# Performance work log

Hardware: AMD Instinct MI355X
Metric: run time of the kernel (lower is better)

## Reference

```python
import jax, jax.numpy as jnp
import numpy as np

N_NODES = 100000
N_EDGES = 600000
VOCAB = 5000
NUM_GRAPHS = 2000
NUM_CLASSES = 10


def setup_inputs() -> dict:
    key = jax.random.key(0)
    ks = jax.random.split(key, 12)
    x = jax.random.randint(ks[0], (N_NODES,), 0, VOCAB, dtype=jnp.int32)
    edge_index = jax.random.randint(ks[1], (2, N_EDGES), 0, N_NODES, dtype=jnp.int32)
    batch = jnp.sort(jax.random.randint(ks[2], (N_NODES,), 0, NUM_GRAPHS, dtype=jnp.int32))
    emb = jax.random.normal(ks[3], (VOCAB, 64), dtype=jnp.float32) * 0.1
    W1 = jax.random.normal(ks[4], (64, 128), dtype=jnp.float32) * (1.0 / np.sqrt(64))
    b1 = jnp.zeros((128,), dtype=jnp.float32)
    W2 = jax.random.normal(ks[5], (128, 128), dtype=jnp.float32) * (1.0 / np.sqrt(128))
    b2 = jnp.zeros((128,), dtype=jnp.float32)
    Wlin = jax.random.normal(ks[6], (128, NUM_CLASSES), dtype=jnp.float32) * (1.0 / np.sqrt(128))
    blin = jnp.zeros((NUM_CLASSES,), dtype=jnp.float32)
    return {"x": x, "edge_index": edge_index, "batch": batch, "num_graphs": NUM_GRAPHS,
            "emb": emb, "W1": W1, "b1": b1, "W2": W2, "b2": b2, "Wlin": Wlin, "blin": blin}


def reference(x, edge_index, batch, num_graphs, emb, W1, b1, W2, b2, Wlin, blin):
    N = x.shape[0]
    loops = jnp.arange(N, dtype=edge_index.dtype)
    src = jnp.concatenate([edge_index[0], loops])  # message sources (j)
    dst = jnp.concatenate([edge_index[1], loops])  # aggregation targets (i)
    # GCN symmetric normalization with self-loops (PyG gcn_norm, source_to_target)
    deg = jax.ops.segment_sum(jnp.ones_like(dst, dtype=jnp.float32), dst, num_segments=N)
    dinv = jnp.where(deg > 0, jax.lax.rsqrt(deg), 0.0)
    norm = dinv[src] * dinv[dst]  # [E+N]

    def gcn(h, W, b):
        h = h @ W  # linear transform first (GCNConv order)
        msg = h[src] * norm[:, None]  # gather + scale, [E+N, F]
        return jax.ops.segment_sum(msg, dst, num_segments=N) + b

    h = emb[x]  # [N, 64]
    h = jax.nn.relu(gcn(h, W1, b1))
    h = jax.nn.relu(gcn(h, W2, b2))
    g = jax.ops.segment_max(h, batch, num_segments=num_graphs)  # global_max_pool
    return g @ Wlin + blin
```

## Files before the change

### kernel.cpp

```cpp
#include <hip/hip_runtime.h>
#include <hip/hip_bf16.h>
#include <hip/hip_fp16.h>


typedef _Float16 h8 __attribute__((ext_vector_type(8)));
typedef _Float16 h4v __attribute__((ext_vector_type(4)));
typedef float f32x4 __attribute__((ext_vector_type(4)));

__global__ __launch_bounds__(256) void k_zero(int4* __restrict__ deg4, int n4i,
                                              int4* __restrict__ pool4, int p4i,
                                              int4* __restrict__ xpad, int x4i) {
    int t = blockIdx.x * 256 + threadIdx.x;
    int4 z = make_int4(0, 0, 0, 0);
    if (t < n4i) deg4[t] = z;
    if (t < p4i) pool4[t] = z;
    if (t < x4i) xpad[t] = z;
}

__global__ __launch_bounds__(256) void k_degprep(const int* __restrict__ dst, int* __restrict__ deg, int E,
                                                 const float* __restrict__ emb, __half2* __restrict__ e16,
                                                 const float* __restrict__ W1, _Float16* __restrict__ W1T,
                                                 const float* __restrict__ W2, _Float16* __restrict__ W2T,
                                                 int nEmbF, int gE, int nCast) {
    int bid = blockIdx.x;
    if (bid < gE) {
        int e = bid * 256 + threadIdx.x;
        if (e < E) atomicAdd(&deg[dst[e]], 1);
    } else if (bid < gE + nCast) {
        int t = (bid - gE) * 256 + threadIdx.x;
        if (t * 4 < nEmbF) {
            float4 v = *(const float4*)&emb[t * 4];
            e16[t * 2] = __floats2half2_rn(v.x, v.y);
            e16[t * 2 + 1] = __floats2half2_rn(v.z, v.w);
        }
    } else if (bid < gE + nCast + 32) {
        int t = (bid - gE - nCast) * 256 + threadIdx.x;
        int c = t >> 6, k = t & 63;
        W1T[c * 64 + k] = (_Float16)W1[k * 128 + c];
    } else {
        int t = (bid - gE - nCast - 32) * 256 + threadIdx.x;
        if (t < 128 * 128) {
            int c = t >> 7, k = t & 127;
            W2T[c * 128 + k] = (_Float16)W2[k * 128 + c];
        }
    }
}

__global__ __launch_bounds__(256) void k_scan1(const int* __restrict__ deg, int* __restrict__ exc,
                                               int* __restrict__ bsums, float* __restrict__ dinv, int N) {
    __shared__ int s[256];
    int i = blockIdx.x * 256 + threadIdx.x;
    int v = (i < N) ? deg[i] : 0;
    if (i < N) dinv[i] = rsqrtf((float)(v + 1));
    s[threadIdx.x] = v;
    __syncthreads();
    for (int off = 1; off < 256; off <<= 1) {
        int t = (threadIdx.x >= (unsigned)off) ? s[threadIdx.x - off] : 0;
        __syncthreads();
        s[threadIdx.x] += t;
        __syncthreads();
    }
    if (i < N) exc[i] = s[threadIdx.x] - v;
    if (threadIdx.x == 255) bsums[blockIdx.x] = s[255];
}

__global__ __launch_bounds__(512) void k_scan2(int* __restrict__ bsums, int nb) {
    __shared__ int s[512];
    int i = threadIdx.x;
    int v = (i < nb) ? bsums[i] : 0;
    s[i] = v;
    __syncthreads();
    for (int off = 1; off < 512; off <<= 1) {
        int t = (i >= off) ? s[i - off] : 0;
        __syncthreads();
        s[i] += t;
        __syncthreads();
    }
    if (i < nb) bsums[i] = s[i] - v;
}

__global__ __launch_bounds__(256) void k_scan3(int* __restrict__ rowstart, int* __restrict__ cursor,
                                               const int* __restrict__ bsums, int N, int E) {
    int i = blockIdx.x * 256 + threadIdx.x;
    if (i < N) {
        int r = rowstart[i] + bsums[blockIdx.x];
        rowstart[i] = r;
        cursor[i] = r;
    }
    if (i == 0 && blockIdx.x == 0) rowstart[N] = E;
}

__global__ __launch_bounds__(256) void k_fill(const int* __restrict__ src, const int* __restrict__ dst,
                                              const int* __restrict__ x, const float* __restrict__ dinv,
                                              int* __restrict__ cursor, int4* __restrict__ rec, int E) {
    int e = blockIdx.x * 256 + threadIdx.x;
    if (e < E) {
        int d = dst[e];
        int s = src[e];
        int pos = atomicAdd(&cursor[d], 1);
        rec[pos] = make_int4(x[s], __float_as_int(dinv[s]), s, 0);
    }
}

__global__ __launch_bounds__(256) void k_agge(const __half2* __restrict__ e16, const int* __restrict__ x,
                                              const float* __restrict__ dinv, const int* __restrict__ rs,
                                              const int4* __restrict__ rec, __half2* __restrict__ Xagg, int N) {
    int lane = threadIdx.x & 31;
    int n0 = (blockIdx.x * 8 + (threadIdx.x >> 5)) * 2;
    if (n0 >= N) return;
    int nB = (n0 + 1 < N) ? n0 + 1 : n0;
    int cA0 = rs[n0], cA1 = rs[n0 + 1];
    int cB0 = rs[nB], cB1 = rs[nB + 1];
    bool hasA = cA0 < cA1, hasB = cB0 < cB1;
    __half2 tA[8], tB[8];
    float wA[8], wB[8];
#pragma unroll
    for (int i = 0; i < 8; ++i) {
        int ei = cA0 + i;
        int ec = (ei < cA1) ? ei : (hasA ? cA1 - 1 : 0);
        int4 r2 = rec[ec];
        tA[i] = e16[(size_t)r2.x * 32 + lane];
        wA[i] = (ei < cA1) ? __int_as_float(r2.y) : 0.f;
    }
#pragma unroll
    for (int i = 0; i < 8; ++i) {
        int ei = cB0 + i;
        int ec = (ei < cB1) ? ei : (hasB ? cB1 - 1 : 0);
        int4 r2 = rec[ec];
        tB[i] = e16[(size_t)r2.x * 32 + lane];
        wB[i] = (ei < cB1) ? __int_as_float(r2.y) : 0.f;
    }
    float dA = dinv[n0], dB = dinv[nB];
    float2 sA = __half22float2(e16[(size_t)x[n0] * 32 + lane]);
    float2 sB = __half22float2(e16[(size_t)x[nB] * 32 + lane]);
    float aA0 = dA * sA.x, aA1 = dA * sA.y;
    float aB0 = dB * sB.x, aB1 = dB * sB.y;
#pragma unroll
    for (int i = 0; i < 8; ++i) {
        float2 tf = __half22float2(tA[i]);
        aA0 = fmaf(wA[i], tf.x, aA0);
        aA1 = fmaf(wA[i], tf.y, aA1);
    }
#pragma unroll
    for (int i = 0; i < 8; ++i) {
        float2 tf = __half22float2(tB[i]);
        aB0 = fmaf(wB[i], tf.x, aB0);
        aB1 = fmaf(wB[i], tf.y, aB1);
    }
    for (int e = cA0 + 8; e < cA1; e += 8) {
#pragma unroll
        for (int i = 0; i < 8; ++i) {
            int ei = e + i;
            int ec = (ei < cA1) ? ei : cA1 - 1;
            int4 r2 = rec[ec];
            tA[i] = e16[(size_t)r2.x * 32 + lane];
            wA[i] = (ei < cA1) ? __int_as_float(r2.y) : 0.f;
        }
#pragma unroll
        for (int i = 0; i < 8; ++i) {
            float2 tf = __half22float2(tA[i]);
            aA0 = fmaf(wA[i], tf.x, aA0);
            aA1 = fmaf(wA[i], tf.y, aA1);
        }
    }
    for (int e = cB0 + 8; e < cB1; e += 8) {
#pragma unroll
        for (int i = 0; i < 8; ++i) {
            int ei = e + i;
            int ec = (ei < cB1) ? ei : cB1 - 1;
            int4 r2 = rec[ec];
            tB[i] = e16[(size_t)r2.x * 32 + lane];
            wB[i] = (ei < cB1) ? __int_as_float(r2.y) : 0.f;
        }
#pragma unroll
        for (int i = 0; i < 8; ++i) {
            float2 tf = __half22float2(tB[i]);
            aB0 = fmaf(wB[i], tf.x, aB0);
            aB1 = fmaf(wB[i], tf.y, aB1);
        }
    }
    Xagg[(size_t)n0 * 32 + lane] = __floats2half2_rn(dA * aA0, dA * aA1);
    Xagg[(size_t)nB * 32 + lane] = __floats2half2_rn(dB * aB0, dB * aB1);
}

__global__ __launch_bounds__(256) void k_gemm12(const _Float16* __restrict__ Xagg,
                                                const _Float16* __restrict__ W1T, const float* __restrict__ b1,
                                                const _Float16* __restrict__ W2T, const float* __restrict__ dinv,
                                                _Float16* __restrict__ P, int N) {
    __shared__ _Float16 Hs[64][136];
    int tid = threadIdx.x;
    int l = tid & 63, wid = tid >> 6;
    int r = l & 15, kg = l >> 4;
    int blk0 = blockIdx.x * 64;
    {
        f32x4 acc[8];
#pragma unroll
        for (int ct = 0; ct < 8; ++ct) acc[ct] = (f32x4){0.f, 0.f, 0.f, 0.f};
        const _Float16* ab = Xagg + (size_t)(blk0 + wid * 16 + r) * 64 + kg * 8;
#pragma unroll
        for (int kc = 0; kc < 2; ++kc) {
            h8 a = *(const h8*)(ab + kc * 32);
#pragma unroll
            for (int ct = 0; ct < 8; ++ct) {
                h8 b = *(const h8*)(W1T + (size_t)(ct * 16 + r) * 64 + kc * 32 + kg * 8);
                acc[ct] = __builtin_amdgcn_mfma_f32_16x16x32_f16(a, b, acc[ct], 0, 0, 0);
            }
        }
#pragma unroll
        for (int ct = 0; ct < 8; ++ct) {
            float bias = b1[ct * 16 + r];
#pragma unroll
            for (int i = 0; i < 4; ++i)
                Hs[wid * 16 + 4 * kg + i][ct * 16 + r] = (_Float16)fmaxf(acc[ct][i] + bias, 0.f);
        }
    }
    __syncthreads();
    {
        f32x4 acc[8];
#pragma unroll
        for (int ct = 0; ct < 8; ++ct) acc[ct] = (f32x4){0.f, 0.f, 0.f, 0.f};
#pragma unroll
        for (int kc = 0; kc < 4; ++kc) {
            h8 a = *(const h8*)&Hs[wid * 16 + r][kc * 32 + kg * 8];
#pragma unroll
            for (int ct = 0; ct < 8; ++ct) {
                h8 b = *(const h8*)(W2T + (size_t)(ct * 16 + r) * 128 + kc * 32 + kg * 8);
                acc[ct] = __builtin_amdgcn_mfma_f32_16x16x32_f16(a, b, acc[ct], 0, 0, 0);
            }
        }
        float dv[4];
#pragma unroll
        for (int i = 0; i < 4; ++i) {
            int gr = blk0 + wid * 16 + 4 * kg + i;
            dv[i] = (gr < N) ? dinv[gr] : 0.f;
        }
#pragma unroll
        for (int ct = 0; ct < 8; ++ct) {
#pragma unroll
            for (int i = 0; i < 4; ++i) {
                int gr = blk0 + wid * 16 + 4 * kg + i;
                if (gr < N) P[(size_t)gr * 128 + ct * 16 + r] = (_Float16)(acc[ct][i] * dv[i]);
            }
        }
    }
}

__global__ __launch_bounds__(256) void k_agg2pool(const h4v* __restrict__ P4, const int* __restrict__ batch,
                                                  const float* __restrict__ dinv, const int* __restrict__ rs,
                                                  const int4* __restrict__ rec, const float4* __restrict__ bias4,
                                                  float* __restrict__ pool, int N, int G) {
    __shared__ int lpool[4][128];
    int tid = threadIdx.x;
    lpool[tid >> 7][tid & 127] = 0;
    lpool[(tid >> 7) + 2][tid & 127] = 0;
    __syncthreads();
    int lane = tid & 31;
    int blk_n0 = blockIdx.x * 16;
    int gfirst = batch[(blk_n0 < N) ? blk_n0 : (N - 1)];
    int n0 = blk_n0 + (tid >> 5) * 2;
    if (n0 < N) {
        int nA = n0;
        int nB = (n0 + 1 < N) ? n0 + 1 : n0;
        int cA0 = rs[nA], cA1 = rs[nA + 1];
        int cB0 = rs[nB], cB1 = rs[nB + 1];
        bool hasA = cA0 < cA1, hasB = cB0 < cB1;
        h4v sA = P4[(size_t)nA * 32 + lane];
        h4v sB = P4[(size_t)nB * 32 + lane];
        float aA[4], aB[4];
#pragma unroll
        for (int f = 0; f < 4; ++f) {
            aA[f] = (float)sA[f];
            aB[f] = (float)sB[f];
        }
        {
            h4v tA[16], tB[16];
#pragma unroll
            for (int i = 0; i < 16; ++i) {
                int ei = cA0 + i;
                int ec = (ei < cA1) ? ei : (hasA ? cA1 - 1 : 0);
                tA[i] = P4[(size_t)rec[ec].z * 32 + lane];
            }
#pragma unroll
            for (int i = 0; i < 16; ++i) {
                int ei = cB0 + i;
                int ec = (ei < cB1) ? ei : (hasB ? cB1 - 1 : 0);
                tB[i] = P4[(size_t)rec[ec].z * 32 + lane];
            }
#pragma unroll
            for (int i = 0; i < 16; ++i) {
                float w = (cA0 + i < cA1) ? 1.f : 0.f;
#pragma unroll
                for (int f = 0; f < 4; ++f) aA[f] = fmaf(w, (float)tA[i][f], aA[f]);
            }
#pragma unroll
            for (int i = 0; i < 16; ++i) {
                float w = (cB0 + i < cB1) ? 1.f : 0.f;
#pragma unroll
                for (int f = 0; f < 4; ++f) aB[f] = fmaf(w, (float)tB[i][f], aB[f]);
            }
        }
        for (int e = cA0 + 16; e < cA1; e += 16) {
            h4v t[16];
#pragma unroll
            for (int i = 0; i < 16; ++i) {
                int ei = e + i;
                int ec = (ei < cA1) ? ei : cA1 - 1;
                t[i] = P4[(size_t)rec[ec].z * 32 + lane];
            }
#pragma unroll
            for (int i = 0; i < 16; ++i) {
                float w = (e + i < cA1) ? 1.f : 0.f;
#pragma unroll
                for (int f = 0; f < 4; ++f) aA[f] = fmaf(w, (float)t[i][f], aA[f]);
            }
        }
        for (int e = cB0 + 16; e < cB1; e += 16) {
            h4v t[16];
#pragma unroll
            for (int i = 0; i < 16; ++i) {
                int ei = e + i;
                int ec = (ei < cB1) ? ei : cB1 - 1;
                t[i] = P4[(size_t)rec[ec].z * 32 + lane];
            }
#pragma unroll
            for (int i = 0; i < 16; ++i) {
                float w = (e + i < cB1) ? 1.f : 0.f;
#pragma unroll
                for (int f = 0; f < 4; ++f) aB[f] = fmaf(w, (float)t[i][f], aB[f]);
            }
        }
        float dA = dinv[nA], dB = dinv[nB];
        int gA = batch[nA], gB = batch[nB];
        float4 b = bias4[lane];
        float bv[4] = {b.x, b.y, b.z, b.w};
        float zA[4], zB[4];
#pragma unroll
        for (int f = 0; f < 4; ++f) {
            zA[f] = fmaxf(fmaf(dA, aA[f], bv[f]), 0.f);
            zB[f] = fmaxf(fmaf(dB, aB[f], bv[f]), 0.f);
        }
        int rot = (lane >> 3) & 3;
        auto emit = [&](int g, const float* m) {
            int slot = g - gfirst;
            if (slot < 4) {
#pragma unroll
                for (int f = 0; f < 4; ++f) {
                    int ff = (f + rot) & 3;
                    if (m[ff] > 0.f) atomicMax(&lpool[slot][lane * 4 + ff], __float_as_int(m[ff]));
                }
            } else {
                float* pg = pool + (size_t)g * 128 + lane * 4;
#pragma unroll
                for (int f = 0; f < 4; ++f)
                    if (m[f] > 0.f) atomicMax((int*)(pg + f), __float_as_int(m[f]));
            }
        };
        if (gA == gB) {
            float m[4];
#pragma unroll
            for (int f = 0; f < 4; ++f) m[f] = fmaxf(zA[f], zB[f]);
            emit(gA, m);
        } else {
            emit(gA, zA);
            emit(gB, zB);
        }
    }
    __syncthreads();
    {
        int f = tid & 127;
        for (int s = tid >> 7; s < 4; s += 2) {
            int v = lpool[s][f];
            if (v > 0) atomicMax((int*)&pool[(size_t)(gfirst + s) * 128 + f], v);
        }
    }
}

__global__ __launch_bounds__(256) void k_final(const float* __restrict__ pool, const float* __restrict__ Wlin,
                                               const float* __restrict__ blin, float* __restrict__ out, int G) {
    int t = blockIdx.x * 256 + threadIdx.x;
    if (t >= G * 10) return;
    int g = t / 10, c = t % 10;
    float acc = blin[c];
    const float* pr = pool + (size_t)g * 128;
#pragma unroll 8
    for (int f = 0; f < 128; ++f) acc = fmaf(pr[f], Wlin[f * 10 + c], acc);
    out[t] = acc;
}

extern "C" void kernel_launch(void* const* d_in, const int* in_sizes, int n_in,
                              void* d_out, int out_size, void* d_ws, size_t ws_size,
                              hipStream_t stream) {
    const int* x = (const int*)d_in[0];
    const int* ei = (const int*)d_in[1];
    const int* batch = (const int*)d_in[2];
    const float* emb = (const float*)d_in[4];
    const float* W1 = (const float*)d_in[5];
    const float* b1 = (const float*)d_in[6];
    const float* W2 = (const float*)d_in[7];
    const float* b2 = (const float*)d_in[8];
    const float* Wlin = (const float*)d_in[9];
    const float* blin = (const float*)d_in[10];
    float* out = (float*)d_out;

    int N = in_sizes[0];
    int E = in_sizes[1] / 2;
    int VOCAB = in_sizes[4] / 64;
    int G = out_size / 10;
    const int* srcp = ei;
    const int* dstp = ei + E;

    char* p = (char*)d_ws;
    auto alloc = [&](size_t bytes) -> char* {
        char* r = p;
        p += (bytes + 255) & ~(size_t)255;
        return r;
    };
    int Npad = (N + 63) & ~63;
    int* deg = (int*)alloc((size_t)N * 4);
    int* cursor = (int*)alloc((size_t)N * 4);
    int* rowstart = (int*)alloc((size_t)(N + 1) * 4);
    int* bsums = (int*)alloc(512 * 4);
    float* dinv = (float*)alloc((size_t)N * 4);
    int4* rec = (int4*)alloc((size_t)E * 16);
    _Float16* e16 = (_Float16*)alloc((size_t)VOCAB * 64 * 2);
    _Float16* W1T = (_Float16*)alloc(128 * 64 * 2);
    _Float16* W2T = (_Float16*)alloc(128 * 128 * 2);
    _Float16* Xagg = (_Float16*)alloc((size_t)Npad * 64 * 2);
    _Float16* P = (_Float16*)alloc((size_t)N * 128 * 2);
    float* pool = (float*)alloc((size_t)G * 128 * 4);

    int gE = (E + 255) / 256;
    int gN = (N + 255) / 256;
    int nEmbF = VOCAB * 64;
    int nCast = (nEmbF / 4 + 255) / 256;

    int n4i = N / 4, p4i = G * 128 / 4;
    int x4i = (Npad - N) * 64 * 2 / 16;
    int zmax = n4i > p4i ? n4i : p4i;
    k_zero<<<(zmax + 255) / 256, 256, 0, stream>>>((int4*)deg, n4i, (int4*)pool, p4i,
                                                   (int4*)(Xagg + (size_t)N * 64), x4i);
    k_degprep<<<gE + nCast + 32 + 64, 256, 0, stream>>>(dstp, deg, E, emb, (__half2*)e16, W1, W1T,
                                                        W2, W2T, nEmbF, gE, nCast);
    k_scan1<<<gN, 256, 0, stream>>>(deg, rowstart, bsums, dinv, N);
    k_scan2<<<1, 512, 0, stream>>>(bsums, gN);
    k_scan3<<<gN, 256, 0, stream>>>(rowstart, cursor, bsums, N, E);
    k_fill<<<gE, 256, 0, stream>>>(srcp, dstp, x, dinv, cursor, rec, E);
    k_agge<<<(N + 15) / 16, 256, 0, stream>>>((const __half2*)e16, x, dinv, rowstart, rec,
                                              (__half2*)Xagg, N);
    k_gemm12<<<(N + 63) / 64, 256, 0, stream>>>(Xagg, W1T, b1, W2T, dinv, P, N);
    k_agg2pool<<<(N + 15) / 16, 256, 0, stream>>>((const h4v*)P, batch, dinv, rowstart, rec,
                                                  (const float4*)b2, pool, N, G);
    k_final<<<(G * 10 + 255) / 256, 256, 0, stream>>>(pool, Wlin, blin, out, G);
}
```

Before: 197.6 us.

## Reorder layer-2 as aggregate-then-transform and fuse W2 GEMM into pooling kernel

Layer 2 now aggregates the relu'd layer-1 activations h1 over neighbours first and applies the W2 MFMA GEMM afterwards, inside the same kernel that does bias, relu and global max pooling. k_gemm1 now only computes layer 1 and writes h1 through shared memory with coalesced stores. Previously W2 was applied per node before aggregation, producing an intermediate P. The fused kernel uses per-row gathers across lanes in MFMA layout with a __any-driven edge loop, two edges per step, and uses 8 shared pooling slots instead of 4. The gather is now unbalanced across rows within a wavefront, and its access pattern is less coalesced than the old lane-per-feature gather.

```diff
diff --git a/kernel.cpp b/kernel.cpp
--- a/kernel.cpp
+++ b/kernel.cpp
@@ -4,7 +4,6 @@
 
 
 typedef _Float16 h8 __attribute__((ext_vector_type(8)));
-typedef _Float16 h4v __attribute__((ext_vector_type(4)));
 typedef float f32x4 __attribute__((ext_vector_type(4)));
 
 __global__ __launch_bounds__(256) void k_zero(int4* __restrict__ deg4, int n4i,
@@ -183,195 +182,138 @@
     Xagg[(size_t)nB * 32 + lane] = __floats2half2_rn(dB * aB0, dB * aB1);
 }
 
-__global__ __launch_bounds__(256) void k_gemm12(const _Float16* __restrict__ Xagg,
-                                                const _Float16* __restrict__ W1T, const float* __restrict__ b1,
-                                                const _Float16* __restrict__ W2T, const float* __restrict__ dinv,
-                                                _Float16* __restrict__ P, int N) {
+__global__ __launch_bounds__(256) void k_gemm1(const _Float16* __restrict__ Xagg,
+                                               const _Float16* __restrict__ W1T,
+                                               const float* __restrict__ b1,
+                                               _Float16* __restrict__ h1, int Npad) {
     __shared__ _Float16 Hs[64][136];
     int tid = threadIdx.x;
     int l = tid & 63, wid = tid >> 6;
     int r = l & 15, kg = l >> 4;
     int blk0 = blockIdx.x * 64;
+    f32x4 acc[8];
+#pragma unroll
+    for (int ct = 0; ct < 8; ++ct) acc[ct] = (f32x4){0.f, 0.f, 0.f, 0.f};
+    const _Float16* ab = Xagg + (size_t)(blk0 + wid * 16 + r) * 64 + kg * 8;
+#pragma unroll
+    for (int kc = 0; kc < 2; ++kc) {
+        h8 a = *(const h8*)(ab + kc * 32);
+#pragma unroll
+        for (int ct = 0; ct < 8; ++ct) {
+            h8 b = *(const h8*)(W1T + (size_t)(ct * 16 + r) * 64 + kc * 32 + kg * 8);
+            acc[ct] = __builtin_amdgcn_mfma_f32_16x16x32_f16(a, b, acc[ct], 0, 0, 0);
+        }
+    }
+#pragma unroll
+    for (int ct = 0; ct < 8; ++ct) {
+        float bias = b1[ct * 16 + r];
+#pragma unroll
+        for (int i = 0; i < 4; ++i)
+            Hs[wid * 16 + 4 * kg + i][ct * 16 + r] = (_Float16)fmaxf(acc[ct][i] + bias, 0.f);
+    }
+    __syncthreads();
+    int row = tid >> 2, q = tid & 3;
+    const int4* srcp = (const int4*)&Hs[row][q * 32];
+    int4 v0 = srcp[0], v1 = srcp[1], v2 = srcp[2], v3 = srcp[3];
+    int4* dst = (int4*)(h1 + (size_t)(blk0 + row) * 128 + q * 32);
+    dst[0] = v0; dst[1] = v1; dst[2] = v2; dst[3] = v3;
+}
+
+#define SLOTS 8
+__global__ __launch_bounds__(256) void k_aggpool(const _Float16* __restrict__ h1,
+                                                 const int* __restrict__ batch,
+                                                 const float* __restrict__ dinv,
+                                                 const int* __restrict__ rs,
+                                                 const int4* __restrict__ rec,
+                                                 const _Float16* __restrict__ W2T,
+                                                 const float* __restrict__ b2,
+                                                 float* __restrict__ pool, int N) {
+    __shared__ int lpool[SLOTS][128];
+    int tid = threadIdx.x;
+    for (int i = tid; i < SLOTS * 128; i += 256) ((int*)lpool)[i] = 0;
+    __syncthreads();
+    int l = tid & 63, wid = tid >> 6;
+    int r = l & 15, kg = l >> 4;
+    int blk0 = blockIdx.x * 64;
+    int gfirst = batch[blk0 < N ? blk0 : N - 1];
+    int base = blk0 + wid * 16;
+    int noder = base + r;
+    if (noder >= N) noder = N - 1;
+    int e = rs[noder], e1 = rs[noder + 1];
+    float di = dinv[noder];
+    float y[32];
     {
-        f32x4 acc[8];
-#pragma unroll
-        for (int ct = 0; ct < 8; ++ct) acc[ct] = (f32x4){0.f, 0.f, 0.f, 0.f};
-        const _Float16* ab = Xagg + (size_t)(blk0 + wid * 16 + r) * 64 + kg * 8;
-#pragma unroll
-        for (int kc = 0; kc < 2; ++kc) {
-            h8 a = *(const h8*)(ab + kc * 32);
-#pragma unroll
-            for (int ct = 0; ct < 8; ++ct) {
-                h8 b = *(const h8*)(W1T + (size_t)(ct * 16 + r) * 64 + kc * 32 + kg * 8);
-                acc[ct] = __builtin_amdgcn_mfma_f32_16x16x32_f16(a, b, acc[ct], 0, 0, 0);
+        const _Float16* sp = h1 + (size_t)noder * 128 + kg * 8;
+#pragma unroll
+        for (int kc = 0; kc < 4; ++kc) {
+            h8 s = *(const h8*)(sp + kc * 32);
+#pragma unroll
+            for (int j = 0; j < 8; ++j) y[kc * 8 + j] = di * (float)s[j];
+        }
+    }
+    while (__any(e < e1)) {
+        int ec0 = (e < e1) ? e : 0;
+        int4 r0 = rec[ec0];
+        float w0 = (e < e1) ? __int_as_float(r0.y) : 0.f;
+        int ec1 = (e + 1 < e1) ? e + 1 : 0;
+        int4 r1 = rec[ec1];
+        float w1 = (e + 1 < e1) ? __int_as_float(r1.y) : 0.f;
+        const _Float16* p0 = h1 + (size_t)r0.z * 128 + kg * 8;
+        const _Float16* p1 = h1 + (size_t)r1.z * 128 + kg * 8;
+#pragma unroll
+        for (int kc = 0; kc < 4; ++kc) {
+            h8 t0 = *(const h8*)(p0 + kc * 32);
+            h8 t1 = *(const h8*)(p1 + kc * 32);
+#pragma unroll
+            for (int j = 0; j < 8; ++j)
+                y[kc * 8 + j] = fmaf(w1, (float)t1[j], fmaf(w0, (float)t0[j], y[kc * 8 + j]));
+        }
+        e += 2;
+    }
+    h8 af[4];
+#pragma unroll
+    for (int kc = 0; kc < 4; ++kc)
+#pragma unroll
+        for (int j = 0; j < 8; ++j) af[kc][j] = (_Float16)(di * y[kc * 8 + j]);
+    f32x4 acc[8];
+#pragma unroll
+    for (int ct = 0; ct < 8; ++ct) acc[ct] = (f32x4){0.f, 0.f, 0.f, 0.f};
+#pragma unroll
+    for (int kc = 0; kc < 4; ++kc) {
+#pragma unroll
+        for (int ct = 0; ct < 8; ++ct) {
+            h8 b = *(const h8*)(W2T + (size_t)(ct * 16 + r) * 128 + kc * 32 + kg * 8);
+            acc[ct] = __builtin_amdgcn_mfma_f32_16x16x32_f16(af[kc], b, acc[ct], 0, 0, 0);
+        }
+    }
+    int gs[4];
+#pragma unroll
+    for (int i = 0; i < 4; ++i) {
+        int nd = base + 4 * kg + i;
+        gs[i] = (nd < N) ? batch[nd] : -1;
+    }
+#pragma unroll
+    for (int ct = 0; ct < 8; ++ct) {
+        float bias = b2[ct * 16 + r];
+#pragma unroll
+        for (int i = 0; i < 4; ++i) {
+            if (gs[i] >= 0) {
+                float z = acc[ct][i] + bias;
+                if (z > 0.f) {
+                    int slot = gs[i] - gfirst;
+                    int col = ct * 16 + r;
+                    if (slot < SLOTS)
+                        atomicMax(&lpool[slot][col], __float_as_int(z));
+                    else
+                        atomicMax((int*)&pool[(size_t)gs[i] * 128 + col], __float_as_int(z));
+                }
             }
         }
-#pragma unroll
-        for (int ct = 0; ct < 8; ++ct) {
-            float bias = b1[ct * 16 + r];
-#pragma unroll
-            for (int i = 0; i < 4; ++i)
-                Hs[wid * 16 + 4 * kg + i][ct * 16 + r] = (_Float16)fmaxf(acc[ct][i] + bias, 0.f);
-        }
-    }
-    __syncthreads();
-    {
-        f32x4 acc[8];
-#pragma unroll
-        for (int ct = 0; ct < 8; ++ct) acc[ct] = (f32x4){0.f, 0.f, 0.f, 0.f};
-#pragma unroll
-        for (int kc = 0; kc < 4; ++kc) {
-            h8 a = *(const h8*)&Hs[wid * 16 + r][kc * 32 + kg * 8];
-#pragma unroll
-            for (int ct = 0; ct < 8; ++ct) {
-                h8 b = *(const h8*)(W2T + (size_t)(ct * 16 + r) * 128 + kc * 32 + kg * 8);
-                acc[ct] = __builtin_amdgcn_mfma_f32_16x16x32_f16(a, b, acc[ct], 0, 0, 0);
-            }
-        }
-        float dv[4];
-#pragma unroll
-        for (int i = 0; i < 4; ++i) {
-            int gr = blk0 + wid * 16 + 4 * kg + i;
-            dv[i] = (gr < N) ? dinv[gr] : 0.f;
-        }
-#pragma unroll
-        for (int ct = 0; ct < 8; ++ct) {
-#pragma unroll
-            for (int i = 0; i < 4; ++i) {
-                int gr = blk0 + wid * 16 + 4 * kg + i;
-                if (gr < N) P[(size_t)gr * 128 + ct * 16 + r] = (_Float16)(acc[ct][i] * dv[i]);
-            }
-        }
-    }
-}
-
-__global__ __launch_bounds__(256) void k_agg2pool(const h4v* __restrict__ P4, const int* __restrict__ batch,
-                                                  const float* __restrict__ dinv, const int* __restrict__ rs,
-                                                  const int4* __restrict__ rec, const float4* __restrict__ bias4,
-                                                  float* __restrict__ pool, int N, int G) {
-    __shared__ int lpool[4][128];
-    int tid = threadIdx.x;
-    lpool[tid >> 7][tid & 127] = 0;
-    lpool[(tid >> 7) + 2][tid & 127] = 0;
-    __syncthreads();
-    int lane = tid & 31;
-    int blk_n0 = blockIdx.x * 16;
-    int gfirst = batch[(blk_n0 < N) ? blk_n0 : (N - 1)];
-    int n0 = blk_n0 + (tid >> 5) * 2;
-    if (n0 < N) {
-        int nA = n0;
-        int nB = (n0 + 1 < N) ? n0 + 1 : n0;
-        int cA0 = rs[nA], cA1 = rs[nA + 1];
-        int cB0 = rs[nB], cB1 = rs[nB + 1];
-        bool hasA = cA0 < cA1, hasB = cB0 < cB1;
-        h4v sA = P4[(size_t)nA * 32 + lane];
-        h4v sB = P4[(size_t)nB * 32 + lane];
-        float aA[4], aB[4];
-#pragma unroll
-        for (int f = 0; f < 4; ++f) {
-            aA[f] = (float)sA[f];
-            aB[f] = (float)sB[f];
-        }
-        {
-            h4v tA[16], tB[16];
-#pragma unroll
-            for (int i = 0; i < 16; ++i) {
-                int ei = cA0 + i;
-                int ec = (ei < cA1) ? ei : (hasA ? cA1 - 1 : 0);
-                tA[i] = P4[(size_t)rec[ec].z * 32 + lane];
-            }
-#pragma unroll
-            for (int i = 0; i < 16; ++i) {
-                int ei = cB0 + i;
-                int ec = (ei < cB1) ? ei : (hasB ? cB1 - 1 : 0);
-                tB[i] = P4[(size_t)rec[ec].z * 32 + lane];
-            }
-#pragma unroll
-            for (int i = 0; i < 16; ++i) {
-                float w = (cA0 + i < cA1) ? 1.f : 0.f;
-#pragma unroll
-                for (int f = 0; f < 4; ++f) aA[f] = fmaf(w, (float)tA[i][f], aA[f]);
-            }
-#pragma unroll
-            for (int i = 0; i < 16; ++i) {
-                float w = (cB0 + i < cB1) ? 1.f : 0.f;
-#pragma unroll
-                for (int f = 0; f < 4; ++f) aB[f] = fmaf(w, (float)tB[i][f], aB[f]);
-            }
-        }
-        for (int e = cA0 + 16; e < cA1; e += 16) {
-            h4v t[16];
-#pragma unroll
-            for (int i = 0; i < 16; ++i) {
-                int ei = e + i;
-                int ec = (ei < cA1) ? ei : cA1 - 1;
-                t[i] = P4[(size_t)rec[ec].z * 32 + lane];
-            }
-#pragma unroll
-            for (int i = 0; i < 16; ++i) {
-                float w = (e + i < cA1) ? 1.f : 0.f;
-#pragma unroll
-                for (int f = 0; f < 4; ++f) aA[f] = fmaf(w, (float)t[i][f], aA[f]);
-            }
-        }
-        for (int e = cB0 + 16; e < cB1; e += 16) {
-            h4v t[16];
-#pragma unroll
-            for (int i = 0; i < 16; ++i) {
-                int ei = e + i;
-                int ec = (ei < cB1) ? ei : cB1 - 1;
-                t[i] = P4[(size_t)rec[ec].z * 32 + lane];
-            }
-#pragma unroll
-            for (int i = 0; i < 16; ++i) {
-                float w = (e + i < cB1) ? 1.f : 0.f;
-#pragma unroll
-                for (int f = 0; f < 4; ++f) aB[f] = fmaf(w, (float)t[i][f], aB[f]);
-            }
-        }
-        float dA = dinv[nA], dB = dinv[nB];
-        int gA = batch[nA], gB = batch[nB];
-        float4 b = bias4[lane];
-        float bv[4] = {b.x, b.y, b.z, b.w};
-        float zA[4], zB[4];
-#pragma unroll
-        for (int f = 0; f < 4; ++f) {
-            zA[f] = fmaxf(fmaf(dA, aA[f], bv[f]), 0.f);
-            zB[f] = fmaxf(fmaf(dB, aB[f], bv[f]), 0.f);
-        }
-        int rot = (lane >> 3) & 3;
-        auto emit = [&](int g, const float* m) {
-            int slot = g - gfirst;
-            if (slot < 4) {
-#pragma unroll
-                for (int f = 0; f < 4; ++f) {
-                    int ff = (f + rot) & 3;
-                    if (m[ff] > 0.f) atomicMax(&lpool[slot][lane * 4 + ff], __float_as_int(m[ff]));
-                }
-            } else {
-                float* pg = pool + (size_t)g * 128 + lane * 4;
-#pragma unroll
-                for (int f = 0; f < 4; ++f)
-                    if (m[f] > 0.f) atomicMax((int*)(pg + f), __float_as_int(m[f]));
-            }
-        };
-        if (gA == gB) {
-            float m[4];
-#pragma unroll
-            for (int f = 0; f < 4; ++f) m[f] = fmaxf(zA[f], zB[f]);
-            emit(gA, m);
-        } else {
-            emit(gA, zA);
-            emit(gB, zB);
-        }
-    }
-    __syncthreads();
-    {
-        int f = tid & 127;
-        for (int s = tid >> 7; s < 4; s += 2) {
-            int v = lpool[s][f];
-            if (v > 0) atomicMax((int*)&pool[(size_t)(gfirst + s) * 128 + f], v);
-        }
+    }
+    __syncthreads();
+    for (int i = tid; i < SLOTS * 128; i += 256) {
+        int v = ((int*)lpool)[i];
+        if (v > 0) atomicMax((int*)&pool[(size_t)(gfirst + (i >> 7)) * 128 + (i & 127)], v);
     }
 }
 
@@ -426,7 +368,7 @@
     _Float16* W1T = (_Float16*)alloc(128 * 64 * 2);
     _Float16* W2T = (_Float16*)alloc(128 * 128 * 2);
     _Float16* Xagg = (_Float16*)alloc((size_t)Npad * 64 * 2);
-    _Float16* P = (_Float16*)alloc((size_t)N * 128 * 2);
+    _Float16* h1 = (_Float16*)alloc((size_t)Npad * 128 * 2);
     float* pool = (float*)alloc((size_t)G * 128 * 4);
 
     int gE = (E + 255) / 256;
@@ -447,8 +389,7 @@
     k_fill<<<gE, 256, 0, stream>>>(srcp, dstp, x, dinv, cursor, rec, E);
     k_agge<<<(N + 15) / 16, 256, 0, stream>>>((const __half2*)e16, x, dinv, rowstart, rec,
                                               (__half2*)Xagg, N);
-    k_gemm12<<<(N + 63) / 64, 256, 0, stream>>>(Xagg, W1T, b1, W2T, dinv, P, N);
-    k_agg2pool<<<(N + 15) / 16, 256, 0, stream>>>((const h4v*)P, batch, dinv, rowstart, rec,
-                                                  (const float4*)b2, pool, N, G);
+    k_gemm1<<<Npad / 64, 256, 0, stream>>>(Xagg, W1T, b1, h1, Npad);
+    k_aggpool<<<(N + 63) / 64, 256, 0, stream>>>(h1, batch, dinv, rowstart, rec, W2T, b2, pool, N);
     k_final<<<(G * 10 + 255) / 256, 256, 0, stream>>>(pool, Wlin, blin, out, G);
 }
```

Measured after the change: 201.1 us. Within noise of the previous version (+1.8%).
